# Kernel optimization log

Measured on AMD Instinct MI355X. Metric: run time of the kernel, lower is better.

The kernel has to match this reference:

```python
import jax, jax.numpy as jnp
import numpy as np

B, S, D, H = 2, 512, 512, 256

def setup_inputs() -> dict:
    key = jax.random.key(0)
    ks = jax.random.split(key, 5)
    x_text = jax.random.normal(ks[0], (B, S, D), dtype=jnp.float32)
    mask = jax.random.randint(ks[1], (B, S), 0, 2, dtype=jnp.int32)
    w1 = jax.random.normal(ks[2], (D, H), dtype=jnp.float32) / np.sqrt(D)
    b1 = jnp.zeros((H,), dtype=jnp.float32)
    w2 = jax.random.normal(ks[3], (D, H), dtype=jnp.float32) / np.sqrt(D)
    b2 = jnp.zeros((H,), dtype=jnp.float32)
    v = jax.random.normal(ks[4], (H,), dtype=jnp.float32) / np.sqrt(H)
    bv = jnp.zeros((), dtype=jnp.float32)
    return {"x_text": x_text, "w1": w1, "b1": b1, "w2": w2, "b2": b2,
            "v": v, "bv": bv, "mask": mask}

def reference(x_text, w1, b1, w2, b2, v, bv, mask):
    # x_attention defaults to x_text.
    a = x_text @ w1 + b1            # W1(x_attention): [B,S,H], broadcast on query dim
    t = x_text @ w2 + b2            # W2(x_text):      [B,S,H], broadcast on key dim
    h = jnp.tanh(a[:, None, :, :] + t[:, :, None, :])   # [B,S,S,H]
    scores = jnp.einsum('bijh,h->bij', h, v) + bv        # V(.): [B,S,S] (trailing 1 squeezed)
    # Faithful softmax_mask: exp, multiply by mask broadcast over dim 1,
    # then 'sum' over the last (size-1) dim -> degenerates to e/(e+eps).
    e = jnp.exp(scores) * mask.astype(scores.dtype)[:, None, :]
    p = e / (e + 1e-16)                                  # [B,S,S]
    out = jnp.einsum('bjd,bij->bid', x_text, p)          # (x_attention * p).sum(-2)
    return out  # return_sequences=True -> [B,S,D]
```

## Files before the change

### kernel.cpp

```cpp
#include <hip/hip_runtime.h>


constexpr int B = 2;
constexpr int S = 512;
constexpr int D = 512;

constexpr int DCHUNKS = 8;
constexpr int ICHUNKS = 16;
constexpr int F4_PER_CHUNK = (D / DCHUNKS) / 4;
constexpr int JLANES = 16;
constexpr int J_PER_LANE = S / JLANES;
constexpr int ROWS_PER_CHUNK = S / ICHUNKS;
constexpr int ROW_F4 = D / 4;

__global__ __launch_bounds__(256)
void attn_masked_colsum_bcast(const float* __restrict__ x,
                              const int* __restrict__ mask,
                              float* __restrict__ out)
{
    __shared__ float4 part[JLANES][F4_PER_CHUNK];

    const int bi  = blockIdx.x;
    const int b   = bi / (ICHUNKS * DCHUNKS);
    const int rem = bi % (ICHUNKS * DCHUNKS);
    const int ic  = rem / DCHUNKS;
    const int dc  = rem % DCHUNKS;

    const int t  = threadIdx.x;
    const int dq = t % F4_PER_CHUNK;
    const int jl = t / F4_PER_CHUNK;

    const float4* xb = (const float4*)(x + (size_t)b * S * D);
    const int dbase_f4 = dc * F4_PER_CHUNK;

    float4 acc = make_float4(0.f, 0.f, 0.f, 0.f);
    #pragma unroll 8
    for (int k = 0; k < J_PER_LANE; ++k) {
        const int j = jl * J_PER_LANE + k;
        const float m = (mask[b * S + j] != 0) ? 1.0f : 0.0f;
        const float4 xv = xb[(size_t)j * ROW_F4 + dbase_f4 + dq];
        acc.x += m * xv.x; acc.y += m * xv.y;
        acc.z += m * xv.z; acc.w += m * xv.w;
    }
    part[jl][dq] = acc;
    __syncthreads();

    if (t < F4_PER_CHUNK) {
        float4 s = part[0][t];
        #pragma unroll
        for (int l = 1; l < JLANES; ++l) {
            const float4 p = part[l][t];
            s.x += p.x; s.y += p.y; s.z += p.z; s.w += p.w;
        }
        part[0][t] = s;
    }
    __syncthreads();

    const float4 cs = part[0][dq];
    float4* outb = (float4*)(out + (size_t)b * S * D);
    const int il0 = t / F4_PER_CHUNK;
    #pragma unroll
    for (int w = 0; w < ROWS_PER_CHUNK / JLANES; ++w) {
        const int i = ic * ROWS_PER_CHUNK + w * JLANES + il0;
        outb[(size_t)i * ROW_F4 + dbase_f4 + dq] = cs;
    }
}

extern "C" void kernel_launch(void* const* d_in, const int* in_sizes, int n_in,
                              void* d_out, int out_size, void* d_ws, size_t ws_size,
                              hipStream_t stream)
{
    const float* x    = (const float*)d_in[0];
    const int*   mask = (const int*)d_in[7];
    float*       out  = (float*)d_out;

    const int grid = B * ICHUNKS * DCHUNKS;
    hipLaunchKernelGGL(attn_masked_colsum_bcast, dim3(grid), dim3(256), 0, stream,
                       x, mask, out);
}
```

Baseline: 68.31 us.

## Split column-sum and broadcast into two kernels to avoid redundant colsum work

Before, each of 256 blocks recomputed the masked column sum over all 512 rows for its D chunk, so every column sum was computed 16 times. Now one kernel computes each column sum once, with 64 blocks each handling 16 columns and using a tree reduction in shared memory, and writes the results to workspace. A second fully parallel kernel then broadcasts them to the output. This removes the redundant reads of x but adds a second launch, a workspace round trip, and runs the colsum with only 64 blocks, each thread making 8 strided 16-byte loads.

After: 70.32 us. +2.9%, slower.

```diff
diff --git a/kernel.cpp b/kernel.cpp
--- a/kernel.cpp
+++ b/kernel.cpp
@@ -4,66 +4,67 @@
 constexpr int B = 2;
 constexpr int S = 512;
 constexpr int D = 512;
-
-constexpr int DCHUNKS = 8;
-constexpr int ICHUNKS = 16;
-constexpr int F4_PER_CHUNK = (D / DCHUNKS) / 4;
-constexpr int JLANES = 16;
-constexpr int J_PER_LANE = S / JLANES;
-constexpr int ROWS_PER_CHUNK = S / ICHUNKS;
 constexpr int ROW_F4 = D / 4;
 
+constexpr int DCH = 32;
+constexpr int F4C = 4;
+constexpr int JL  = 64;
+constexpr int JPL = S / JL;
+
 __global__ __launch_bounds__(256)
-void attn_masked_colsum_bcast(const float* __restrict__ x,
-                              const int* __restrict__ mask,
-                              float* __restrict__ out)
+void colsum_kernel(const float* __restrict__ x,
+                   const int* __restrict__ mask,
+                   float* __restrict__ ws)
 {
-    __shared__ float4 part[JLANES][F4_PER_CHUNK];
+    __shared__ float4 part[JL][F4C];
 
-    const int bi  = blockIdx.x;
-    const int b   = bi / (ICHUNKS * DCHUNKS);
-    const int rem = bi % (ICHUNKS * DCHUNKS);
-    const int ic  = rem / DCHUNKS;
-    const int dc  = rem % DCHUNKS;
-
+    const int b  = blockIdx.x / DCH;
+    const int dc = blockIdx.x % DCH;
     const int t  = threadIdx.x;
-    const int dq = t % F4_PER_CHUNK;
-    const int jl = t / F4_PER_CHUNK;
+    const int dq = t & (F4C - 1);
+    const int jl = t >> 2;
 
     const float4* xb = (const float4*)(x + (size_t)b * S * D);
-    const int dbase_f4 = dc * F4_PER_CHUNK;
+    const int f4 = dc * F4C + dq;
 
     float4 acc = make_float4(0.f, 0.f, 0.f, 0.f);
-    #pragma unroll 8
-    for (int k = 0; k < J_PER_LANE; ++k) {
-        const int j = jl * J_PER_LANE + k;
+    #pragma unroll
+    for (int k = 0; k < JPL; ++k) {
+        const int j = jl * JPL + k;
         const float m = (mask[b * S + j] != 0) ? 1.0f : 0.0f;
-        const float4 xv = xb[(size_t)j * ROW_F4 + dbase_f4 + dq];
+        const float4 xv = xb[(size_t)j * ROW_F4 + f4];
         acc.x += m * xv.x; acc.y += m * xv.y;
         acc.z += m * xv.z; acc.w += m * xv.w;
     }
     part[jl][dq] = acc;
     __syncthreads();
 
-    if (t < F4_PER_CHUNK) {
-        float4 s = part[0][t];
-        #pragma unroll
-        for (int l = 1; l < JLANES; ++l) {
-            const float4 p = part[l][t];
+    #pragma unroll
+    for (int off = JL / 2; off >= 1; off >>= 1) {
+        if (jl < off) {
+            const float4 p = part[jl + off][dq];
+            float4 s = part[jl][dq];
             s.x += p.x; s.y += p.y; s.z += p.z; s.w += p.w;
+            part[jl][dq] = s;
         }
-        part[0][t] = s;
+        __syncthreads();
     }
-    __syncthreads();
 
-    const float4 cs = part[0][dq];
-    float4* outb = (float4*)(out + (size_t)b * S * D);
-    const int il0 = t / F4_PER_CHUNK;
-    #pragma unroll
-    for (int w = 0; w < ROWS_PER_CHUNK / JLANES; ++w) {
-        const int i = ic * ROWS_PER_CHUNK + w * JLANES + il0;
-        outb[(size_t)i * ROW_F4 + dbase_f4 + dq] = cs;
+    if (t < F4C) {
+        float4* cs = (float4*)ws;
+        cs[b * ROW_F4 + f4] = part[0][t];
     }
+}
+
+__global__ __launch_bounds__(256)
+void bcast_kernel(const float* __restrict__ ws,
+                  float* __restrict__ out)
+{
+    const int idx = blockIdx.x * 256 + threadIdx.x;
+    const int b   = idx / (S * ROW_F4);
+    const int d4  = idx & (ROW_F4 - 1);
+    const float4* cs = (const float4*)ws;
+    ((float4*)out)[idx] = cs[b * ROW_F4 + d4];
 }
 
 extern "C" void kernel_launch(void* const* d_in, const int* in_sizes, int n_in,
@@ -73,8 +74,10 @@
     const float* x    = (const float*)d_in[0];
     const int*   mask = (const int*)d_in[7];
     float*       out  = (float*)d_out;
+    float*       ws   = (float*)d_ws;
 
-    const int grid = B * ICHUNKS * DCHUNKS;
-    hipLaunchKernelGGL(attn_masked_colsum_bcast, dim3(grid), dim3(256), 0, stream,
-                       x, mask, out);
+    hipLaunchKernelGGL(colsum_kernel, dim3(B * DCH), dim3(256), 0, stream,
+                       x, mask, ws);
+    hipLaunchKernelGGL(bcast_kernel, dim3((B * S * ROW_F4) / 256), dim3(256), 0, stream,
+                       ws, out);
 }
```
